# Kernel optimization log

Measured on AMD Instinct MI355X. Metric: run time of the kernel, lower is better.

## Reference

```python
import jax, jax.numpy as jnp
import numpy as np


def setup_inputs() -> dict:
    key = jax.random.key(0)
    k1, k2 = jax.random.split(key)
    B, N, M, C = 32, 4096, 4096, 3
    xyz1 = jax.random.normal(k1, (B, N, C), dtype=jnp.float32)
    xyz2 = jax.random.normal(k2, (B, M, C), dtype=jnp.float32)
    return {"xyz1": xyz1, "xyz2": xyz2}


def _chamfer_l2(xyz1, xyz2):
    # Pairwise squared L2 distances via ||a||^2 + ||b||^2 - 2 a.b  (b n m)
    sq1 = jnp.sum(xyz1 * xyz1, axis=-1)            # [B, N]
    sq2 = jnp.sum(xyz2 * xyz2, axis=-1)            # [B, M]
    cross = jnp.einsum('bnc,bmc->bnm', xyz1, xyz2) # [B, N, M]
    d = sq1[:, :, None] + sq2[:, None, :] - 2.0 * cross
    dist1 = jnp.min(d, axis=2)                     # [B, N] nearest in xyz2
    dist2 = jnp.min(d, axis=1)                     # [B, M] nearest in xyz1
    return jnp.mean(dist1, axis=-1) + jnp.mean(dist2, axis=-1)  # [B]


def reference(xyz1, xyz2):
    return _chamfer_l2(xyz1, xyz2)
```

## Files before the change

kernel.cpp:

```cpp
#include <hip/hip_runtime.h>

typedef _Float16 half8 __attribute__((ext_vector_type(8)));
typedef float floatx16 __attribute__((ext_vector_type(16)));

#define TPB    256
#define QPB    512
#define CHUNK  1024
#define NTILE  (CHUNK / 32)
#define SMH    (CHUNK * 16)


#define FMIN __builtin_fminf

__device__ __forceinline__ float fold16(floatx16 d) {
    float m0 = FMIN(FMIN(d[0],  d[1]),  d[2]);
    float m1 = FMIN(FMIN(d[3],  d[4]),  d[5]);
    float m2 = FMIN(FMIN(d[6],  d[7]),  d[8]);
    float m3 = FMIN(FMIN(d[9],  d[10]), d[11]);
    float m4 = FMIN(FMIN(d[12], d[13]), d[14]);
    float n0 = FMIN(FMIN(m0, m1), m2);
    float n1 = FMIN(FMIN(m3, m4), d[15]);
    return FMIN(n0, n1);
}

__device__ __forceinline__ void wr_point(_Float16* __restrict__ smb, int j,
                                         float x, float y, float z) {
    float hq = 0.5f * (x * x + y * y + z * z);
    _Float16 xh = (_Float16)x, yh = (_Float16)y, zh = (_Float16)z;
    _Float16 xl = (_Float16)(x - (float)xh);
    _Float16 yl = (_Float16)(y - (float)yh);
    _Float16 zl = (_Float16)(z - (float)zh);
    _Float16 qh = (_Float16)hq;
    _Float16 ql = (_Float16)(hq - (float)qh);
    const _Float16 hz = (_Float16)0.0f;
    int t = j >> 5, c = j & 31;
    half8 v0, v1;
    v0[0] = xh; v0[1] = xl; v0[2] = xh; v0[3] = yh;
    v0[4] = yl; v0[5] = yh; v0[6] = zh; v0[7] = zl;
    v1[0] = zh; v1[1] = qh; v1[2] = ql; v1[3] = hz;
    v1[4] = hz; v1[5] = hz; v1[6] = hz; v1[7] = hz;
    *(half8*)&smb[t * 512 + c * 8]       = v0;
    *(half8*)&smb[t * 512 + 256 + c * 8] = v1;
}

__global__ __launch_bounds__(TPB, 4) void chamfer_mfma(const float* __restrict__ xyz1,
                                                       const float* __restrict__ xyz2,
                                                       float* __restrict__ ws,
                                                       int N, int M, int QCAP,
                                                       int nchunks) {
    const int b = blockIdx.y, dir = blockIdx.z;
    const int B = gridDim.y;
    const int qblock = (int)blockIdx.x / nchunks;
    const int chunk  = (int)blockIdx.x % nchunks;
    const float* __restrict__ P = dir ? xyz2 + (size_t)b * M * 3 : xyz1 + (size_t)b * N * 3;
    const float* __restrict__ Q = dir ? xyz1 + (size_t)b * N * 3 : xyz2 + (size_t)b * M * 3;
    const int nq = dir ? M : N;
    const int md = dir ? N : M;

    if (qblock * QPB >= nq) return;

    const int base = chunk * CHUNK;

    __shared__ __align__(16) _Float16 smB[SMH];

    const int tid = (int)threadIdx.x;
    const int w   = tid >> 6;
    const int l   = tid & 63;
    const int m   = l & 31;
    const int h   = l >> 5;

    const _Float16 hz = (_Float16)0.0f, hone = (_Float16)1.0f;
    const int qb = qblock * QPB + w * 128;

    half8 qfr[4];
#pragma unroll
    for (int g = 0; g < 4; ++g) {
        int idx = qb + g * 32 + m;
        int ci  = idx < nq ? idx : nq - 1;
        float x = P[3 * ci], y = P[3 * ci + 1], z = P[3 * ci + 2];
        _Float16 xh = (_Float16)x, yh = (_Float16)y, zh = (_Float16)z;
        _Float16 xl = (_Float16)(x - (float)xh);
        _Float16 yl = (_Float16)(y - (float)yh);
        _Float16 zl = (_Float16)(z - (float)zh);
        half8 a;
        if (h == 0) {
            a[0] = -xh; a[1] = -xh; a[2] = -xl; a[3] = -yh;
            a[4] = -yh; a[5] = -yl; a[6] = -zh; a[7] = -zh;
        } else {
            a[0] = -zl; a[1] = hone; a[2] = hone; a[3] = hz;
            a[4] = hz;  a[5] = hz;   a[6] = hz;  a[7] = hz;
        }
        qfr[g] = a;
    }

    {
        int g0 = base + tid;
        int g1 = base + tid + 256;
        int g2 = base + tid + 512;
        int g3 = base + tid + 768;
        g0 = g0 < md ? g0 : md - 1;
        g1 = g1 < md ? g1 : md - 1;
        g2 = g2 < md ? g2 : md - 1;
        g3 = g3 < md ? g3 : md - 1;
        float x0 = Q[3 * g0], y0 = Q[3 * g0 + 1], z0 = Q[3 * g0 + 2];
        float x1 = Q[3 * g1], y1 = Q[3 * g1 + 1], z1 = Q[3 * g1 + 2];
        float x2 = Q[3 * g2], y2 = Q[3 * g2 + 1], z2 = Q[3 * g2 + 2];
        float x3 = Q[3 * g3], y3 = Q[3 * g3 + 1], z3 = Q[3 * g3 + 2];
        wr_point(smB, tid,       x0, y0, z0);
        wr_point(smB, tid + 256, x1, y1, z1);
        wr_point(smB, tid + 512, x2, y2, z2);
        wr_point(smB, tid + 768, x3, y3, z3);
    }
    __syncthreads();

    float rmq0 = 3.0e38f, rmq1 = 3.0e38f;
    float rmq2 = 3.0e38f, rmq3 = 3.0e38f;

    const floatx16 czero = {0.0f, 0.0f, 0.0f, 0.0f, 0.0f, 0.0f, 0.0f, 0.0f,
                            0.0f, 0.0f, 0.0f, 0.0f, 0.0f, 0.0f, 0.0f, 0.0f};

    const _Float16* bp = &smB[h * 256 + m * 8];
    half8 cur = *(const half8*)(bp);
#pragma unroll 1
    for (int t = 0; t < NTILE; ++t) {
        half8 nx = *(const half8*)(bp + ((t + 1) & (NTILE - 1)) * 512);
        floatx16 d0 = __builtin_amdgcn_mfma_f32_32x32x16_f16(cur, qfr[0], czero, 0, 0, 0);
        floatx16 d1 = __builtin_amdgcn_mfma_f32_32x32x16_f16(cur, qfr[1], czero, 0, 0, 0);
        rmq0 = FMIN(rmq0, fold16(d0));
        floatx16 d2 = __builtin_amdgcn_mfma_f32_32x32x16_f16(cur, qfr[2], czero, 0, 0, 0);
        rmq1 = FMIN(rmq1, fold16(d1));
        floatx16 d3 = __builtin_amdgcn_mfma_f32_32x32x16_f16(cur, qfr[3], czero, 0, 0, 0);
        rmq2 = FMIN(rmq2, fold16(d2));
        rmq3 = FMIN(rmq3, fold16(d3));
        cur = nx;
    }

    rmq0 = FMIN(rmq0, __shfl_xor(rmq0, 32, 64));
    rmq1 = FMIN(rmq1, __shfl_xor(rmq1, 32, 64));
    rmq2 = FMIN(rmq2, __shfl_xor(rmq2, 32, 64));
    rmq3 = FMIN(rmq3, __shfl_xor(rmq3, 32, 64));

    float* __restrict__ wsd = ws + (((size_t)chunk * 2 + dir) * B + b) * QCAP;
    const int ia = qb + h * 64 + m;
    const int ib = ia + 32;
    const float va = h ? rmq2 : rmq0;
    const float vb = h ? rmq3 : rmq1;
    if (ia < nq) wsd[ia] = va;
    if (ib < nq) wsd[ib] = vb;
}

__global__ __launch_bounds__(256) void chamfer_reduce(const float* __restrict__ xyz1,
                                                      const float* __restrict__ xyz2,
                                                      const float* __restrict__ ws,
                                                      float* __restrict__ out,
                                                      int N, int M, int QCAP,
                                                      int nchunks) {
    const int b = (int)blockIdx.x, dir = (int)blockIdx.y;
    const int B = gridDim.x;
    const float* __restrict__ P = dir ? xyz2 + (size_t)b * M * 3 : xyz1 + (size_t)b * N * 3;
    const int nq = dir ? M : N;
    const size_t cs = (size_t)2 * B * QCAP;
    const float* __restrict__ w0 = ws + ((size_t)dir * B + b) * QCAP;

    float s = 0.0f;
    for (int q = (int)threadIdx.x + (int)blockIdx.z * 256; q < nq; q += 256 * (int)gridDim.z) {
        float v = w0[q];
        for (int c = 1; c < nchunks; ++c) v = FMIN(v, w0[c * cs + q]);
        float x = P[3 * q], y = P[3 * q + 1], z = P[3 * q + 2];
        s += v + 0.5f * (x * x + y * y + z * z);
    }
#pragma unroll
    for (int off = 32; off > 0; off >>= 1) s += __shfl_down(s, off, 64);
    __shared__ float red[4];
    if ((threadIdx.x & 63) == 0) red[threadIdx.x >> 6] = s;
    __syncthreads();
    if (threadIdx.x == 0) {
        float t = (red[0] + red[1]) + (red[2] + red[3]);
        atomicAdd(out + b, t * (2.0f / (float)nq));
    }
}

extern "C" void kernel_launch(void* const* d_in, const int* in_sizes, int n_in,
                              void* d_out, int out_size, void* d_ws, size_t ws_size,
                              hipStream_t stream) {
    const float* xyz1 = (const float*)d_in[0];
    const float* xyz2 = (const float*)d_in[1];
    float* out = (float*)d_out;

    const int B = out_size;
    const int N = in_sizes[0] / (3 * B);
    const int M = in_sizes[1] / (3 * B);

    hipMemsetAsync(d_out, 0, (size_t)B * sizeof(float), stream);

    const int qmax    = N > M ? N : M;
    const int qblocks = (qmax + QPB - 1) / QPB;
    const int QCAP    = ((qmax + 255) / 256) * 256;
    const int nchunks = (qmax + CHUNK - 1) / CHUNK;

    dim3 grid(qblocks * nchunks, B, 2);
    chamfer_mfma<<<grid, dim3(TPB), 0, stream>>>(xyz1, xyz2, (float*)d_ws, N, M, QCAP, nchunks);
    chamfer_reduce<<<dim3(B, 2, 4), dim3(256), 0, stream>>>(xyz1, xyz2, (float*)d_ws, out, N, M, QCAP, nchunks);
}
```

Measured before the change: 96.75 us.

## Keep elementwise min accumulators across tiles and halve queries per block

Instead of folding each 16-element MFMA result to a scalar every tile, the kernel keeps two 16-wide vector min accumulators and folds them once after the loop. This cuts per-tile reduction work from about 15 min ops per MFMA to 16 independent mins. To limit register growth, each wave now handles 64 queries instead of 128, which doubles the grid and the number of times each B chunk is staged into shared memory. The output write mapping changes to match.

```diff
diff --git a/kernel.cpp b/kernel.cpp
--- a/kernel.cpp
+++ b/kernel.cpp
@@ -4,13 +4,19 @@
 typedef float floatx16 __attribute__((ext_vector_type(16)));
 
 #define TPB    256
-#define QPB    512
+#define QPB    256
 #define CHUNK  1024
 #define NTILE  (CHUNK / 32)
 #define SMH    (CHUNK * 16)
 
 
 #define FMIN __builtin_fminf
+
+__device__ __forceinline__ floatx16 vmin16(floatx16 a, floatx16 d) {
+#pragma unroll
+    for (int i = 0; i < 16; ++i) a[i] = FMIN(a[i], d[i]);
+    return a;
+}
 
 __device__ __forceinline__ float fold16(floatx16 d) {
     float m0 = FMIN(FMIN(d[0],  d[1]),  d[2]);
@@ -70,11 +76,11 @@
     const int h   = l >> 5;
 
     const _Float16 hz = (_Float16)0.0f, hone = (_Float16)1.0f;
-    const int qb = qblock * QPB + w * 128;
-
-    half8 qfr[4];
-#pragma unroll
-    for (int g = 0; g < 4; ++g) {
+    const int qb = qblock * QPB + w * 64;
+
+    half8 qfr[2];
+#pragma unroll
+    for (int g = 0; g < 2; ++g) {
         int idx = qb + g * 32 + m;
         int ci  = idx < nq ? idx : nq - 1;
         float x = P[3 * ci], y = P[3 * ci + 1], z = P[3 * ci + 2];
@@ -113,11 +119,11 @@
     }
     __syncthreads();
 
-    float rmq0 = 3.0e38f, rmq1 = 3.0e38f;
-    float rmq2 = 3.0e38f, rmq3 = 3.0e38f;
-
     const floatx16 czero = {0.0f, 0.0f, 0.0f, 0.0f, 0.0f, 0.0f, 0.0f, 0.0f,
                             0.0f, 0.0f, 0.0f, 0.0f, 0.0f, 0.0f, 0.0f, 0.0f};
+    floatx16 rv0, rv1;
+#pragma unroll
+    for (int i = 0; i < 16; ++i) { rv0[i] = 3.0e38f; rv1[i] = 3.0e38f; }
 
     const _Float16* bp = &smB[h * 256 + m * 8];
     half8 cur = *(const half8*)(bp);
@@ -126,27 +132,20 @@
         half8 nx = *(const half8*)(bp + ((t + 1) & (NTILE - 1)) * 512);
         floatx16 d0 = __builtin_amdgcn_mfma_f32_32x32x16_f16(cur, qfr[0], czero, 0, 0, 0);
         floatx16 d1 = __builtin_amdgcn_mfma_f32_32x32x16_f16(cur, qfr[1], czero, 0, 0, 0);
-        rmq0 = FMIN(rmq0, fold16(d0));
-        floatx16 d2 = __builtin_amdgcn_mfma_f32_32x32x16_f16(cur, qfr[2], czero, 0, 0, 0);
-        rmq1 = FMIN(rmq1, fold16(d1));
-        floatx16 d3 = __builtin_amdgcn_mfma_f32_32x32x16_f16(cur, qfr[3], czero, 0, 0, 0);
-        rmq2 = FMIN(rmq2, fold16(d2));
-        rmq3 = FMIN(rmq3, fold16(d3));
+        rv0 = vmin16(rv0, d0);
+        rv1 = vmin16(rv1, d1);
         cur = nx;
     }
 
+    float rmq0 = fold16(rv0);
+    float rmq1 = fold16(rv1);
     rmq0 = FMIN(rmq0, __shfl_xor(rmq0, 32, 64));
     rmq1 = FMIN(rmq1, __shfl_xor(rmq1, 32, 64));
-    rmq2 = FMIN(rmq2, __shfl_xor(rmq2, 32, 64));
-    rmq3 = FMIN(rmq3, __shfl_xor(rmq3, 32, 64));
 
     float* __restrict__ wsd = ws + (((size_t)chunk * 2 + dir) * B + b) * QCAP;
-    const int ia = qb + h * 64 + m;
-    const int ib = ia + 32;
-    const float va = h ? rmq2 : rmq0;
-    const float vb = h ? rmq3 : rmq1;
-    if (ia < nq) wsd[ia] = va;
-    if (ib < nq) wsd[ib] = vb;
+    const int idx = qb + l;
+    const float val = h ? rmq1 : rmq0;
+    if (idx < nq) wsd[idx] = val;
 }
 
 __global__ __launch_bounds__(256) void chamfer_reduce(const float* __restrict__ xyz1,
```

Result: slower. 162.0 us (+67.5%).
